# Kernel tuning notes

Hardware: AMD Instinct MI355X
Metric: run time of the kernel (lower is better)

Reference implementation:

```python
import jax, jax.numpy as jnp
import numpy as np

NUM_HEADS = 16
HEAD_DIM = 64
WINDOW = 512
D_MODEL = NUM_HEADS * HEAD_DIM
BATCH = 2
SEQ = 2048


def setup_inputs() -> dict:
    key = jax.random.key(0)
    k1, k2, k3 = jax.random.split(key, 3)
    x = jax.random.normal(k1, (BATCH, SEQ, D_MODEL), dtype=jnp.float32)
    # Dense layer params (lecun_normal-like scale for stability)
    qkv_kernel = jax.random.normal(k2, (D_MODEL, 3 * NUM_HEADS * HEAD_DIM), dtype=jnp.float32) / np.sqrt(D_MODEL)
    qkv_bias = jnp.zeros((3 * NUM_HEADS * HEAD_DIM,), dtype=jnp.float32)
    out_kernel = jax.random.normal(k3, (NUM_HEADS * HEAD_DIM, D_MODEL), dtype=jnp.float32) / np.sqrt(D_MODEL)
    out_bias = jnp.zeros((D_MODEL,), dtype=jnp.float32)
    return {"x": x, "qkv_kernel": qkv_kernel, "qkv_bias": qkv_bias,
            "out_kernel": out_kernel, "out_bias": out_bias}


def reference(x, qkv_kernel, qkv_bias, out_kernel, out_bias):
    b, s, d = x.shape
    qkv = x @ qkv_kernel + qkv_bias                       # (b, s, 3*H*hd)
    qkv = qkv.reshape(b, s, 3, NUM_HEADS, HEAD_DIM)
    q = qkv[:, :, 0].transpose(0, 2, 1, 3)                # (b, H, s, hd)
    k = qkv[:, :, 1].transpose(0, 2, 1, 3)
    v = qkv[:, :, 2].transpose(0, 2, 1, 3)
    scale = 1.0 / jnp.sqrt(jnp.float32(HEAD_DIM)).astype(x.dtype)
    scores = jnp.einsum('bhqd,bhkd->bhqk', q, k) * scale  # (b, H, s, s)
    rows = jnp.arange(s)[:, None]
    cols = jnp.arange(s)[None, :]
    window_mask = (rows - cols >= 0) & (rows - cols < WINDOW)
    scores = jnp.where(window_mask[None, None], scores, jnp.asarray(-1e9, scores.dtype))
    attn = jax.nn.softmax(scores, axis=-1)
    out = jnp.einsum('bhqk,bhkd->bhqd', attn, v)          # (b, H, s, hd)
    out = out.transpose(0, 2, 1, 3).reshape(b, s, -1)
    return out @ out_kernel + out_bias
```

## Files before the change

### kernel.cpp

```cpp
#include <hip/hip_runtime.h>
#include <cstdint>
#include <cstddef>

#define NUM_HEADS 16
#define HEAD_DIM  64
#define WINDOW    512
#define D_MODEL   1024
#define BATCH     2
#define SEQ       2048
#define MTOT      (BATCH*SEQ)
#define NQKV      (3*D_MODEL)

typedef short bf16x8 __attribute__((ext_vector_type(8)));
typedef float f32x4  __attribute__((ext_vector_type(4)));

__device__ __forceinline__ f32x4 mfma16(bf16x8 a, bf16x8 b, f32x4 c) {
  return __builtin_amdgcn_mfma_f32_16x16x32_bf16(a, b, c, 0, 0, 0);
}

__device__ __forceinline__ unsigned short f2bf(float f) {
  unsigned int u = __float_as_uint(f);
  u += 0x7fffu + ((u >> 16) & 1u);
  return (unsigned short)(u >> 16);
}
__device__ __forceinline__ float bf2f(unsigned short b) {
  return __uint_as_float(((unsigned int)b) << 16);
}

__device__ __forceinline__ void gld16(const unsigned short* g, unsigned short* l) {
  __builtin_amdgcn_global_load_lds(
      (const __attribute__((address_space(1))) unsigned int*)g,
      (__attribute__((address_space(3))) unsigned int*)l, 16, 0, 0);
}

__global__ __launch_bounds__(256) void prep_kernel(const float* __restrict__ x,
                                                   const float* __restrict__ qkv_w,
                                                   const float* __restrict__ out_w,
                                                   unsigned short* __restrict__ Xb,
                                                   unsigned short* __restrict__ Wq,
                                                   unsigned short* __restrict__ Wo) {
  __shared__ float tile[32][33];
  const int bid = blockIdx.x, t = threadIdx.x;
  if (bid < 4096) {
    int i = (bid * 256 + t) * 4;
    float4 v = *(const float4*)(x + i);
    ushort4 o;
    o.x = f2bf(v.x); o.y = f2bf(v.y); o.z = f2bf(v.z); o.w = f2bf(v.w);
    *(ushort4*)(Xb + i) = o;
    return;
  }
  const float* in; unsigned short* out; int R, C, bx, by;
  if (bid < 7168) { int b2 = bid - 4096; in = qkv_w; out = Wq; R = D_MODEL; C = NQKV; bx = b2 % 96; by = b2 / 96; }
  else            { int b2 = bid - 7168; in = out_w; out = Wo; R = D_MODEL; C = D_MODEL; bx = b2 & 31; by = b2 >> 5; }
  int tx = t & 31, ty = t >> 5;
  int c0 = bx * 32, r0 = by * 32;
#pragma unroll
  for (int i = 0; i < 32; i += 8)
    tile[ty + i][tx] = in[(size_t)(r0 + ty + i) * C + c0 + tx];
  __syncthreads();
#pragma unroll
  for (int i = 0; i < 32; i += 8)
    out[(size_t)(c0 + ty + i) * R + r0 + tx] = f2bf(tile[tx][ty + i]);
}

template<bool SWAP, int K>
__device__ __forceinline__ void gemm_mainloop512(const unsigned short* __restrict__ A,
                                                 const unsigned short* __restrict__ Bt,
                                                 int m0, int n0,
                                                 unsigned short* sA, unsigned short* sB,
                                                 f32x4 (&acc)[2][4]) {
  const int t = threadIdx.x;
  const int lane = t & 63, wave = t >> 6;
  const int wr = wave >> 1, wc = wave & 1;
  const int lhi = lane >> 4, llo = lane & 15;
  f32x4 zero = {0.f, 0.f, 0.f, 0.f};
#pragma unroll
  for (int i = 0; i < 2; ++i)
#pragma unroll
    for (int j = 0; j < 4; ++j) acc[i][j] = zero;

  const int cswz = (((t & 3) ^ ((t >> 3) & 3)) << 3);
  const unsigned short* gA = A  + (size_t)(m0 + (t >> 2)) * K + cswz;
  const unsigned short* gB = Bt + (size_t)(n0 + (t >> 2)) * K + cswz;
  const int ldsT = t * 8;
  const int rsw  = (lhi ^ ((llo >> 1) & 3)) * 8;
  const int aoff = (wr * 32 + llo) * 32 + rsw;
  const int boff = (wc * 64 + llo) * 32 + rsw;
  constexpr int nIter = K / 32;

  auto stage = [&](int s) {
    unsigned short* dA = sA + (s % 3) * 4096;
    unsigned short* dB = sB + (s % 3) * 4096;
    gld16(gA + s * 32, dA + ldsT);
    gld16(gB + s * 32, dB + ldsT);
  };

  stage(0);
  stage(1);
#pragma unroll
  for (int it = 0; it < nIter; ++it) {
    if (it + 1 < nIter) asm volatile("s_waitcnt vmcnt(2)\n\ts_barrier" ::: "memory");
    else                asm volatile("s_waitcnt vmcnt(0)\n\ts_barrier" ::: "memory");
    if (it + 2 < nIter) stage(it + 2);
    const unsigned short* cA = sA + (it % 3) * 4096;
    const unsigned short* cB = sB + (it % 3) * 4096;
    bf16x8 af[2], bfr[4];
#pragma unroll
    for (int i = 0; i < 2; ++i) af[i]  = *(const bf16x8*)(cA + aoff + i * 512);
#pragma unroll
    for (int j = 0; j < 4; ++j)  bfr[j] = *(const bf16x8*)(cB + boff + j * 512);
#pragma unroll
    for (int i = 0; i < 2; ++i)
#pragma unroll
      for (int j = 0; j < 4; ++j)
        acc[i][j] = SWAP ? mfma16(bfr[j], af[i], acc[i][j])
                         : mfma16(af[i], bfr[j], acc[i][j]);
  }
}

template<bool SWAP>
__device__ __forceinline__ void gemm_mainloop_256sq(const unsigned short* __restrict__ A,
                                                    const unsigned short* __restrict__ Bt,
                                                    int m0, int n0,
                                                    unsigned short* sA, unsigned short* sB,
                                                    f32x4 (&acc)[8][4]) {
  constexpr int K  = D_MODEL;
  constexpr int nT = K / 32;
  const int t = threadIdx.x;
  const int lane = t & 63, wave = t >> 6;
  const int wr = wave >> 2, wc = wave & 3;
  const int lhi = lane >> 4, llo = lane & 15;
  f32x4 zero = {0.f, 0.f, 0.f, 0.f};
#pragma unroll
  for (int i = 0; i < 8; ++i)
#pragma unroll
    for (int j = 0; j < 4; ++j) acc[i][j] = zero;

  const int cswz = (((t & 3) ^ ((t >> 3) & 3)) << 3);
  const unsigned short* gA0 = A  + (size_t)(m0 + (t >> 2)) * K + cswz;
  const unsigned short* gA1 = gA0 + (size_t)128 * K;
  const unsigned short* gB0 = Bt + (size_t)(n0 + (t >> 2)) * K + cswz;
  const unsigned short* gB1 = gB0 + (size_t)128 * K;
  const int ldsT0 = t * 8, ldsT1 = 4096 + t * 8;

  const int rsw  = (lhi ^ ((llo >> 1) & 3)) * 8;
  const int aoff = (wr * 128 + llo) * 32 + rsw;
  const int boff = (wc * 64  + llo) * 32 + rsw;

  auto stageA = [&](int tile) {
    unsigned short* d = sA + (tile & 3) * 8192;
    gld16(gA0 + tile * 32, d + ldsT0);
    gld16(gA1 + tile * 32, d + ldsT1);
  };
  auto stageB = [&](int tile) {
    unsigned short* d = sB + (tile & 3) * 8192;
    gld16(gB0 + tile * 32, d + ldsT0);
    gld16(gB1 + tile * 32, d + ldsT1);
  };

  auto compute = [&](int tile, bool prefetch) {
    const unsigned short* cA = sA + (tile & 3) * 8192;
    const unsigned short* cB = sB + (tile & 3) * 8192;
#pragma unroll
    for (int mh = 0; mh < 2; ++mh) {
      if (prefetch) { if (mh == 0) stageA(tile + 2); else stageB(tile + 2); }
      bf16x8 af[4], bfr[4];
#pragma unroll
      for (int i = 0; i < 4; ++i) af[i]  = *(const bf16x8*)(cA + aoff + (mh * 4 + i) * 512);
#pragma unroll
      for (int j = 0; j < 4; ++j) bfr[j] = *(const bf16x8*)(cB + boff + j * 512);
      __builtin_amdgcn_s_setprio(1);
#pragma unroll
      for (int i = 0; i < 4; ++i)
#pragma unroll
        for (int j = 0; j < 4; ++j)
          acc[mh * 4 + i][j] = SWAP ? mfma16(bfr[j], af[i], acc[mh * 4 + i][j])
                                    : mfma16(af[i], bfr[j], acc[mh * 4 + i][j]);
      __builtin_amdgcn_s_setprio(0);
      if (mh == 0) __builtin_amdgcn_s_barrier();
    }
  };

  stageA(0); stageB(0); stageA(1); stageB(1);

  for (int tile = 0; tile < nT - 2; ++tile) {
    asm volatile("s_waitcnt vmcnt(4)\n\ts_barrier" ::: "memory");
    compute(tile, true);
  }
  asm volatile("s_waitcnt vmcnt(4)\n\ts_barrier" ::: "memory");
  compute(nT - 2, false);
  asm volatile("s_waitcnt vmcnt(0)\n\ts_barrier" ::: "memory");
  compute(nT - 1, false);
}

__global__ __launch_bounds__(512, 2) void qkv_gemm_kernel(const unsigned short* __restrict__ Xb,
                                                          const unsigned short* __restrict__ Wt,
                                                          const float* __restrict__ bias,
                                                          unsigned short* __restrict__ Qw,
                                                          unsigned short* __restrict__ Kw,
                                                          unsigned short* __restrict__ Vtw) {
  __shared__ __align__(16) unsigned short sA[4][256 * 32];
  __shared__ __align__(16) unsigned short sB[4][256 * 32];
  f32x4 acc[8][4];
  const int m0 = blockIdx.y * 256, n0 = blockIdx.x * 256;
  const int t = threadIdx.x, lane = t & 63, wave = t >> 6;
  const int wr = wave >> 2, wc = wave & 3, lhi = lane >> 4, llo = lane & 15;

  if (n0 < 2048) {
    gemm_mainloop_256sq<false>(Xb, Wt, m0, n0, sA[0], sB[0], acc);
    const int c = n0 >> 10;
    unsigned short* __restrict__ Dst = (c == 0) ? Qw : Kw;
    const float qs = (c == 0) ? 0.125f : 1.0f;
#pragma unroll
    for (int mi = 0; mi < 8; ++mi) {
#pragma unroll
      for (int nj = 0; nj < 4; ++nj) {
        int n = n0 + wc * 64 + nj * 16 + llo;
        float bv = bias[n];
        int h = (n >> 6) & 15, d = n & 63;
#pragma unroll
        for (int r = 0; r < 4; ++r) {
          int m = m0 + wr * 128 + mi * 16 + lhi * 4 + r;
          int b = m >> 11, s = m & 2047;
          int bh = b * 16 + h;
          Dst[((size_t)(bh * 2048 + s)) * 64 + d] = f2bf((acc[mi][nj][r] + bv) * qs);
        }
      }
    }
  } else {
    gemm_mainloop_256sq<true>(Xb, Wt, m0, n0, sA[0], sB[0], acc);
#pragma unroll
    for (int mi = 0; mi < 8; ++mi) {
      int m = m0 + wr * 128 + mi * 16 + llo;
      int b = m >> 11, s = m & 2047;
#pragma unroll
      for (int nj = 0; nj < 4; ++nj) {
        int nb = n0 + wc * 64 + nj * 16 + lhi * 4;
        float4 bv = *(const float4*)(bias + nb);
        int h = (nb >> 6) & 15, dbase = nb & 63;
        int bh = b * 16 + h;
        float bvr[4] = {bv.x, bv.y, bv.z, bv.w};
#pragma unroll
        for (int r = 0; r < 4; ++r)
          Vtw[(size_t)(bh * 64 + dbase + r) * 2048 + s] = f2bf(acc[mi][nj][r] + bvr[r]);
      }
    }
  }
}

__global__ __launch_bounds__(512) void attn_kernel(const unsigned short* __restrict__ Qw,
                                                   const unsigned short* __restrict__ Kw,
                                                   const unsigned short* __restrict__ Vtw,
                                                   unsigned short* __restrict__ AO) {
  __shared__ __align__(16) unsigned short sK[3][64 * 64];
  __shared__ __align__(16) unsigned short sV[3][64 * 64];
  __shared__ __align__(16) unsigned short sP[8][16 * 72];
  const int t = threadIdx.x, lane = t & 63, wave = t >> 6;
  const int lhi = lane >> 4, llo = lane & 15;
  const int bh = blockIdx.x;
  const int q0 = (15 - blockIdx.y) << 7;
  const unsigned short* Qb = Qw  + (size_t)bh * 2048 * 64;
  const unsigned short* Kb = Kw  + (size_t)bh * 2048 * 64;
  const unsigned short* Vb = Vtw + (size_t)bh * 64 * 2048;

  const int qw = q0 + wave * 16;
  const int qrow = qw + llo;
  bf16x8 qf0 = *(const bf16x8*)(Qb + (size_t)qrow * 64 + lhi * 8);
  bf16x8 qf1 = *(const bf16x8*)(Qb + (size_t)qrow * 64 + 32 + lhi * 8);

  const int srow = t >> 3;
  const int scol = ((t & 7) ^ (srow & 7)) * 8;
  const int cpos  = (lhi ^ (llo & 7)) * 8;
  const int cposx = cpos ^ 32;

  float m_i = -1e30f, l_i = 0.f;
  f32x4 o[4];
  f32x4 zero = {0.f, 0.f, 0.f, 0.f};
#pragma unroll
  for (int td = 0; td < 4; ++td) o[td] = zero;

  const int kt_lo = (q0 > 511) ? ((q0 - 511) >> 6) : 0;
  const int kt_hi = (q0 + 127) >> 6;

  auto stageKV = [&](int j) {
    const int k0 = j << 6;
    unsigned short* dK = sK[j % 3];
    unsigned short* dV = sV[j % 3];
    gld16(Kb + (size_t)(k0 + srow) * 64 + scol, dK + t * 8);
    gld16(Vb + (size_t)srow * 2048 + k0 + scol, dV + t * 8);
  };

  stageKV(kt_lo);
  stageKV(kt_lo + 1);

  for (int kt = kt_lo; kt <= kt_hi; ++kt) {
    if (kt < kt_hi) asm volatile("s_waitcnt vmcnt(2)\n\ts_barrier" ::: "memory");
    else            asm volatile("s_waitcnt vmcnt(0)\n\ts_barrier" ::: "memory");
    if (kt + 2 <= kt_hi) stageKV(kt + 2);
    const int k0 = kt << 6;
    if (k0 > qw + 15 || k0 + 63 < qw - (WINDOW - 1)) continue;

    const unsigned short* bK = sK[kt % 3];
    const unsigned short* bV = sV[kt % 3];

    f32x4 st[4];
#pragma unroll
    for (int tk = 0; tk < 4; ++tk) {
      const unsigned short* kr = bK + (tk * 16 + llo) * 64;
      bf16x8 kf0 = *(const bf16x8*)(kr + cpos);
      bf16x8 kf1 = *(const bf16x8*)(kr + cposx);
      f32x4 z = zero;
      z = mfma16(kf0, qf0, z);
      z = mfma16(kf1, qf1, z);
      st[tk] = z;
    }

    const bool interior = (k0 >= qw - (WINDOW - 1 - 15)) && (k0 + 63 <= qw);
    const int kb = k0 + lhi * 4;
    float mx = -1e30f;
    if (interior) {
#pragma unroll
      for (int tk = 0; tk < 4; ++tk)
#pragma unroll
        for (int r = 0; r < 4; ++r) mx = fmaxf(mx, st[tk][r]);
    } else {
#pragma unroll
      for (int tk = 0; tk < 4; ++tk)
#pragma unroll
        for (int r = 0; r < 4; ++r) {
          int key = kb + tk * 16 + r;
          bool ok = (key <= qrow) && (qrow - key < WINDOW);
          float s = ok ? st[tk][r] : -1e30f;
          st[tk][r] = s;
          mx = fmaxf(mx, s);
        }
    }
    mx = fmaxf(mx, __shfl_xor(mx, 16));
    mx = fmaxf(mx, __shfl_xor(mx, 32));
    float mn = fmaxf(m_i, mx);
    float a  = __expf(m_i - mn);
    float rs = 0.f;
    unsigned short* pw = &sP[wave][llo * 72];
#pragma unroll
    for (int tk = 0; tk < 4; ++tk) {
      ushort4 pb;
      pb.x = f2bf(__expf(st[tk][0] - mn));
      pb.y = f2bf(__expf(st[tk][1] - mn));
      pb.z = f2bf(__expf(st[tk][2] - mn));
      pb.w = f2bf(__expf(st[tk][3] - mn));
      *(ushort4*)(pw + tk * 16 + lhi * 4) = pb;
      rs += bf2f(pb.x) + bf2f(pb.y) + bf2f(pb.z) + bf2f(pb.w);
    }
    rs += __shfl_xor(rs, 16);
    rs += __shfl_xor(rs, 32);
    l_i = l_i * a + rs;
    m_i = mn;

    float aR[4];
#pragma unroll
    for (int r = 0; r < 4; ++r) aR[r] = __shfl(a, lhi * 4 + r);
#pragma unroll
    for (int td = 0; td < 4; ++td)
#pragma unroll
      for (int r = 0; r < 4; ++r) o[td][r] *= aR[r];

    bf16x8 pf0 = *(const bf16x8*)(pw + lhi * 8);
    bf16x8 pf1 = *(const bf16x8*)(pw + 32 + lhi * 8);
#pragma unroll
    for (int td = 0; td < 4; ++td) {
      const unsigned short* vr = bV + (td * 16 + llo) * 64;
      bf16x8 vf0 = *(const bf16x8*)(vr + cpos);
      bf16x8 vf1 = *(const bf16x8*)(vr + cposx);
      o[td] = mfma16(pf0, vf0, o[td]);
      o[td] = mfma16(pf1, vf1, o[td]);
    }
  }

  float lR[4];
#pragma unroll
  for (int r = 0; r < 4; ++r) lR[r] = 1.f / __shfl(l_i, lhi * 4 + r);
  const int b = bh >> 4, h = bh & 15;
#pragma unroll
  for (int td = 0; td < 4; ++td)
#pragma unroll
    for (int r = 0; r < 4; ++r) {
      int qr = q0 + wave * 16 + lhi * 4 + r;
      AO[(size_t)(b * 2048 + qr) * 1024 + h * 64 + td * 16 + llo] = f2bf(o[td][r] * lR[r]);
    }
}

__global__ __launch_bounds__(512, 2) void out_gemm_kernel(const unsigned short* __restrict__ AO,
                                                          const unsigned short* __restrict__ Wt,
                                                          const float* __restrict__ bias,
                                                          float* __restrict__ out) {
  __shared__ __align__(16) unsigned short sA[3][128 * 32];
  __shared__ __align__(16) unsigned short sB[3][128 * 32];
  f32x4 acc[2][4];
  const int m0 = blockIdx.y * 128, n0 = blockIdx.x * 128;
  gemm_mainloop512<false, D_MODEL>(AO, Wt, m0, n0, sA[0], sB[0], acc);

  const int t = threadIdx.x, lane = t & 63, wave = t >> 6;
  const int wr = wave >> 1, wc = wave & 1, lhi = lane >> 4, llo = lane & 15;
#pragma unroll
  for (int ti = 0; ti < 2; ++ti)
#pragma unroll
    for (int tj = 0; tj < 4; ++tj) {
      int n = n0 + wc * 64 + tj * 16 + llo;
      float bv = bias[n];
#pragma unroll
      for (int r = 0; r < 4; ++r) {
        int m = m0 + wr * 32 + ti * 16 + lhi * 4 + r;
        out[(size_t)m * D_MODEL + n] = acc[ti][tj][r] + bv;
      }
    }
}

extern "C" void kernel_launch(void* const* d_in, const int* in_sizes, int n_in,
                              void* d_out, int out_size, void* d_ws, size_t ws_size,
                              hipStream_t stream) {
  const float* x      = (const float*)d_in[0];
  const float* qkv_w  = (const float*)d_in[1];
  const float* qkv_b  = (const float*)d_in[2];
  const float* out_w  = (const float*)d_in[3];
  const float* out_b  = (const float*)d_in[4];
  float* out = (float*)d_out;
  char* ws = (char*)d_ws;

  unsigned short* Xb  = (unsigned short*)(ws);
  unsigned short* Wq  = (unsigned short*)(ws + ((size_t)8  << 20));
  unsigned short* Wo  = (unsigned short*)(ws + ((size_t)14 << 20));
  unsigned short* Qw  = (unsigned short*)(ws + ((size_t)16 << 20));
  unsigned short* Kw  = (unsigned short*)(ws + ((size_t)24 << 20));
  unsigned short* Vtw = (unsigned short*)(ws + ((size_t)32 << 20));
  unsigned short* AO  = (unsigned short*)(ws + ((size_t)40 << 20));

  prep_kernel<<<8192, 256, 0, stream>>>(x, qkv_w, out_w, Xb, Wq, Wo);
  qkv_gemm_kernel<<<dim3(NQKV / 256, MTOT / 256), 512, 0, stream>>>(Xb, Wq, qkv_b, Qw, Kw, Vtw);
  attn_kernel<<<dim3(BATCH * NUM_HEADS, SEQ / 128), 512, 0, stream>>>(Qw, Kw, Vtw, AO);
  out_gemm_kernel<<<dim3(D_MODEL / 128, MTOT / 128), 512, 0, stream>>>(AO, Wo, out_b, out);
}
```

Measured before the change: 174.7 us.

## Restructure QKV GEMM mainloop into K=64 quadrant phases with finer prefetch

The QKV projection GEMM mainloop now steps K in 64-wide tiles instead of 32 and splits each 256x256 tile into four 128x128 quadrant phases. Each phase issues one quadrant's loads for the next tile and waits at a barrier before its MFMAs, so global-to-LDS staging interleaves more finely with compute. LDS is reorganized into double-buffered quadrant slabs with a new XOR swizzle, and the wave-to-row mapping changes. The aim is to halve the outer iterations and hide memory latency better, at the cost of more barriers and more intricate vmcnt bookkeeping.

```diff
diff --git a/kernel.cpp b/kernel.cpp
--- a/kernel.cpp
+++ b/kernel.cpp
@@ -119,15 +119,14 @@
 }
 
 template<bool SWAP>
-__device__ __forceinline__ void gemm_mainloop_256sq(const unsigned short* __restrict__ A,
-                                                    const unsigned short* __restrict__ Bt,
-                                                    int m0, int n0,
-                                                    unsigned short* sA, unsigned short* sB,
-                                                    f32x4 (&acc)[8][4]) {
-  constexpr int K  = D_MODEL;
-  constexpr int nT = K / 32;
-  const int t = threadIdx.x;
-  const int lane = t & 63, wave = t >> 6;
+__device__ __forceinline__ void gemm_mainloop_256q(const unsigned short* __restrict__ A,
+                                                   const unsigned short* __restrict__ Bt,
+                                                   int m0, int n0,
+                                                   unsigned short* sA, unsigned short* sB,
+                                                   f32x4 (&acc)[8][4]) {
+  constexpr int K = D_MODEL;
+  constexpr int nT = K / 64;
+  const int t = threadIdx.x, lane = t & 63, wave = t >> 6;
   const int wr = wave >> 2, wc = wave & 3;
   const int lhi = lane >> 4, llo = lane & 15;
   f32x4 zero = {0.f, 0.f, 0.f, 0.f};
@@ -136,61 +135,78 @@
 #pragma unroll
     for (int j = 0; j < 4; ++j) acc[i][j] = zero;
 
-  const int cswz = (((t & 3) ^ ((t >> 3) & 3)) << 3);
-  const unsigned short* gA0 = A  + (size_t)(m0 + (t >> 2)) * K + cswz;
-  const unsigned short* gA1 = gA0 + (size_t)128 * K;
-  const unsigned short* gB0 = Bt + (size_t)(n0 + (t >> 2)) * K + cswz;
-  const unsigned short* gB1 = gB0 + (size_t)128 * K;
-  const int ldsT0 = t * 8, ldsT1 = 4096 + t * 8;
-
-  const int rsw  = (lhi ^ ((llo >> 1) & 3)) * 8;
-  const int aoff = (wr * 128 + llo) * 32 + rsw;
-  const int boff = (wc * 64  + llo) * 32 + rsw;
-
-  auto stageA = [&](int tile) {
-    unsigned short* d = sA + (tile & 3) * 8192;
-    gld16(gA0 + tile * 32, d + ldsT0);
-    gld16(gA1 + tile * 32, d + ldsT1);
+  const int r6 = t >> 3;
+  const int chunkS = (t & 7) ^ (r6 & 7);
+  const unsigned short* gAr = A  + (size_t)(m0 + r6) * K + chunkS * 8;
+  const unsigned short* gBr = Bt + (size_t)(n0 + (r6 >> 5) * 64 + (r6 & 31)) * K + chunkS * 8;
+  const int dstT = t * 8;
+
+  const int k0off = (lhi ^ (llo & 7)) * 8;
+  const int k1off = k0off ^ 32;
+  const int aRow = (wr * 64 + llo) * 64;
+  const int bRow = (wc * 32 + llo) * 64;
+
+  auto stA = [&](int j, int mh) {
+    unsigned short* d = sA + (((j & 1) << 1) + mh) * 8192 + dstT;
+    const unsigned short* g = gAr + (size_t)(mh * 64) * K + j * 64;
+    gld16(g, d);
+    gld16(g + (size_t)128 * K, d + 4096);
   };
-  auto stageB = [&](int tile) {
-    unsigned short* d = sB + (tile & 3) * 8192;
-    gld16(gB0 + tile * 32, d + ldsT0);
-    gld16(gB1 + tile * 32, d + ldsT1);
+  auto stB = [&](int j, int nh) {
+    unsigned short* d = sB + (((j & 1) << 1) + nh) * 8192 + dstT;
+    const unsigned short* g = gBr + (size_t)(nh * 32) * K + j * 64;
+    gld16(g, d);
+    gld16(g + (size_t)128 * K, d + 4096);
   };
 
-  auto compute = [&](int tile, bool prefetch) {
-    const unsigned short* cA = sA + (tile & 3) * 8192;
-    const unsigned short* cB = sB + (tile & 3) * 8192;
-#pragma unroll
-    for (int mh = 0; mh < 2; ++mh) {
-      if (prefetch) { if (mh == 0) stageA(tile + 2); else stageB(tile + 2); }
-      bf16x8 af[4], bfr[4];
-#pragma unroll
-      for (int i = 0; i < 4; ++i) af[i]  = *(const bf16x8*)(cA + aoff + (mh * 4 + i) * 512);
-#pragma unroll
-      for (int j = 0; j < 4; ++j) bfr[j] = *(const bf16x8*)(cB + boff + j * 512);
-      __builtin_amdgcn_s_setprio(1);
-#pragma unroll
-      for (int i = 0; i < 4; ++i)
-#pragma unroll
-        for (int j = 0; j < 4; ++j)
-          acc[mh * 4 + i][j] = SWAP ? mfma16(bfr[j], af[i], acc[mh * 4 + i][j])
-                                    : mfma16(af[i], bfr[j], acc[mh * 4 + i][j]);
-      __builtin_amdgcn_s_setprio(0);
-      if (mh == 0) __builtin_amdgcn_s_barrier();
-    }
-  };
-
-  stageA(0); stageB(0); stageA(1); stageB(1);
-
-  for (int tile = 0; tile < nT - 2; ++tile) {
-    asm volatile("s_waitcnt vmcnt(4)\n\ts_barrier" ::: "memory");
-    compute(tile, true);
+#define QPHASE(JV, MH, NH, STG)                                                  \
+  {                                                                              \
+    const unsigned short* cA = sA + ((((JV) & 1) << 1) + (MH)) * 8192;           \
+    const unsigned short* cB = sB + ((((JV) & 1) << 1) + (NH)) * 8192;           \
+    bf16x8 af[4][2], bfv[2][2];                                                  \
+    _Pragma("unroll") for (int i2 = 0; i2 < 4; ++i2) {                           \
+      af[i2][0] = *(const bf16x8*)(cA + aRow + i2 * 1024 + k0off);               \
+      af[i2][1] = *(const bf16x8*)(cA + aRow + i2 * 1024 + k1off);               \
+    }                                                                            \
+    _Pragma("unroll") for (int j2 = 0; j2 < 2; ++j2) {                           \
+      bfv[j2][0] = *(const bf16x8*)(cB + bRow + j2 * 1024 + k0off);              \
+      bfv[j2][1] = *(const bf16x8*)(cB + bRow + j2 * 1024 + k1off);              \
+    }                                                                            \
+    STG;                                                                         \
+    asm volatile("s_barrier" ::: "memory");                                      \
+    __builtin_amdgcn_s_setprio(1);                                               \
+    _Pragma("unroll") for (int i2 = 0; i2 < 4; ++i2)                             \
+      _Pragma("unroll") for (int j2 = 0; j2 < 2; ++j2) {                         \
+        f32x4& ac = acc[(MH) * 4 + i2][(NH) * 2 + j2];                           \
+        ac = SWAP ? mfma16(bfv[j2][0], af[i2][0], ac)                            \
+                  : mfma16(af[i2][0], bfv[j2][0], ac);                           \
+        ac = SWAP ? mfma16(bfv[j2][1], af[i2][1], ac)                            \
+                  : mfma16(af[i2][1], bfv[j2][1], ac);                           \
+      }                                                                          \
+    __builtin_amdgcn_s_setprio(0);                                               \
+  }
+
+  stA(0, 0); stB(0, 0); stB(0, 1); stA(0, 1); stA(1, 0);
+
+  for (int j = 0; j < nT - 1; ++j) {
+    asm volatile("s_waitcnt vmcnt(6)\n\ts_barrier" ::: "memory");
+    QPHASE(j, 0, 0, { stB(j + 1, 0); });
+    asm volatile("s_waitcnt vmcnt(6)\n\ts_barrier" ::: "memory");
+    QPHASE(j, 0, 1, { stB(j + 1, 1); });
+    asm volatile("s_waitcnt vmcnt(6)\n\ts_barrier" ::: "memory");
+    QPHASE(j, 1, 0, { stA(j + 1, 1); });
+    asm volatile("s_waitcnt vmcnt(6)\n\ts_barrier" ::: "memory");
+    QPHASE(j, 1, 1, { if (j + 2 < nT) stA(j + 2, 0); });
   }
   asm volatile("s_waitcnt vmcnt(4)\n\ts_barrier" ::: "memory");
-  compute(nT - 2, false);
+  QPHASE(nT - 1, 0, 0, {});
+  asm volatile("s_waitcnt vmcnt(2)\n\ts_barrier" ::: "memory");
+  QPHASE(nT - 1, 0, 1, {});
   asm volatile("s_waitcnt vmcnt(0)\n\ts_barrier" ::: "memory");
-  compute(nT - 1, false);
+  QPHASE(nT - 1, 1, 0, {});
+  asm volatile("s_barrier" ::: "memory");
+  QPHASE(nT - 1, 1, 1, {});
+#undef QPHASE
 }
 
 __global__ __launch_bounds__(512, 2) void qkv_gemm_kernel(const unsigned short* __restrict__ Xb,
@@ -199,15 +215,15 @@
                                                           unsigned short* __restrict__ Qw,
                                                           unsigned short* __restrict__ Kw,
                                                           unsigned short* __restrict__ Vtw) {
-  __shared__ __align__(16) unsigned short sA[4][256 * 32];
-  __shared__ __align__(16) unsigned short sB[4][256 * 32];
+  __shared__ __align__(16) unsigned short sA[2 * 2 * 8192];
+  __shared__ __align__(16) unsigned short sB[2 * 2 * 8192];
   f32x4 acc[8][4];
   const int m0 = blockIdx.y * 256, n0 = blockIdx.x * 256;
   const int t = threadIdx.x, lane = t & 63, wave = t >> 6;
   const int wr = wave >> 2, wc = wave & 3, lhi = lane >> 4, llo = lane & 15;
 
   if (n0 < 2048) {
-    gemm_mainloop_256sq<false>(Xb, Wt, m0, n0, sA[0], sB[0], acc);
+    gemm_mainloop_256q<false>(Xb, Wt, m0, n0, sA, sB, acc);
     const int c = n0 >> 10;
     unsigned short* __restrict__ Dst = (c == 0) ? Qw : Kw;
     const float qs = (c == 0) ? 0.125f : 1.0f;
@@ -228,7 +244,7 @@
       }
     }
   } else {
-    gemm_mainloop_256sq<true>(Xb, Wt, m0, n0, sA[0], sB[0], acc);
+    gemm_mainloop_256q<true>(Xb, Wt, m0, n0, sA, sB, acc);
 #pragma unroll
     for (int mi = 0; mi < 8; ++mi) {
       int m = m0 + wr * 128 + mi * 16 + llo;
```

Measured after the change: 169.0 us. -3.2%, faster.
